# Kernel optimization log

Measured on AMD Instinct MI355X. Metric: run time of the kernel, lower is better.

## Reference

```python
import jax, jax.numpy as jnp
import numpy as np

DIM_IN = 1024
DIM_OUT = 1024


def setup_inputs() -> dict:
    key = jax.random.key(0)
    k1, k2, k3, k4 = jax.random.split(key, 4)
    X = jax.random.normal(k1, (4, 2048, DIM_IN), dtype=jnp.float32)
    s = 1.0 / np.sqrt(DIM_IN)
    Wq = jax.random.normal(k2, (DIM_IN, DIM_OUT), dtype=jnp.float32) * s
    Wk = jax.random.normal(k3, (DIM_IN, DIM_OUT), dtype=jnp.float32) * s
    Wv = jax.random.normal(k4, (DIM_IN, DIM_OUT), dtype=jnp.float32) * s
    return {"X": X, "Wq": Wq, "Wk": Wk, "Wv": Wv}


def reference(X, Wq, Wk, Wv):
    # X: [B, T, Din]; projections (qkv_bias=False)
    q = jnp.einsum('btd,de->bte', X, Wq)   # [B, T, Dout]
    k = jnp.einsum('btd,de->bte', X, Wk)
    v = jnp.einsum('btd,de->bte', X, Wv)
    T = X.shape[1]
    scores = jnp.einsum('bqe,bke->bqk', q, k)  # [B, T, T]
    causal = jnp.tril(jnp.ones((T, T), dtype=bool))  # mask upper triangle (future)
    scores = jnp.where(causal, scores, -jnp.inf)
    # scale=True: divide by sqrt(d); -inf stays -inf so order vs mask is irrelevant
    scores = scores / jnp.sqrt(jnp.asarray(k.shape[-1], dtype=scores.dtype))
    weights = jax.nn.softmax(scores, axis=-1)
    # dropout p=0.0 -> identity
    return jnp.einsum('bqk,bke->bqe', weights, v)
```

## Files before the change

### kernel.cpp

```cpp
#include <hip/hip_runtime.h>
#include <hip/hip_bf16.h>

typedef unsigned short u16;
typedef __bf16 bf16x8 __attribute__((ext_vector_type(8)));
typedef float f32x4 __attribute__((ext_vector_type(4)));
typedef unsigned short u16x8 __attribute__((ext_vector_type(8)));
typedef unsigned short u16x4 __attribute__((ext_vector_type(4)));

__device__ __forceinline__ float bf2f(u16 u) {
  unsigned int x = ((unsigned int)u) << 16;
  return __builtin_bit_cast(float, x);
}
__device__ __forceinline__ u16 f2bf(float f) {
  unsigned int x = __builtin_bit_cast(unsigned int, f);
  x = x + 0x7FFFu + ((x >> 16) & 1u);
  return (u16)(x >> 16);
}

__device__ __forceinline__ void gload_lds16(const u16* g, u16* l) {
  __builtin_amdgcn_global_load_lds(
      (const __attribute__((address_space(1))) unsigned int*)(unsigned long long)(uintptr_t)g,
      (__attribute__((address_space(3))) unsigned int*)(unsigned int)(uintptr_t)l,
      16, 0, 0);
}

__global__ __launch_bounds__(256) void prep_kernel(const float* __restrict__ X,
                                                   const float* __restrict__ Wq,
                                                   const float* __restrict__ Wk,
                                                   const float* __restrict__ Wv,
                                                   u16* __restrict__ Xb,
                                                   u16* __restrict__ Wt) {
  const int id = blockIdx.x;
  const int tid = threadIdx.x;
  if (id < 4096) {
    long i = ((long)id * 256 + tid) * 8;
    float4 a = *reinterpret_cast<const float4*>(X + i);
    float4 b = *reinterpret_cast<const float4*>(X + i + 4);
    u16x8 o;
    o[0] = f2bf(a.x); o[1] = f2bf(a.y); o[2] = f2bf(a.z); o[3] = f2bf(a.w);
    o[4] = f2bf(b.x); o[5] = f2bf(b.y); o[6] = f2bf(b.z); o[7] = f2bf(b.w);
    *reinterpret_cast<u16x8*>(Xb + i) = o;
    return;
  }
  __shared__ u16 t[64][72];
  const int id2 = id - 4096;
  const int z = id2 >> 8;
  const float* W = (z == 0) ? Wq : (z == 1) ? Wk : Wv;
  const float scale = (z == 0) ? (1.0f / 32.0f) : 1.0f;
  u16* out = Wt + (long)z * 1048576;
  const int c0 = (id2 & 15) * 64;
  const int r0 = ((id2 >> 4) & 15) * 64;
#pragma unroll
  for (int i = 0; i < 4; ++i) {
    int slot = tid + 256 * i;
    int lr = slot >> 4;
    int lc4 = slot & 15;
    float4 v = *reinterpret_cast<const float4*>(W + (long)(r0 + lr) * 1024 + c0 + lc4 * 4);
    t[lr][lc4 * 4 + 0] = f2bf(v.x * scale);
    t[lr][lc4 * 4 + 1] = f2bf(v.y * scale);
    t[lr][lc4 * 4 + 2] = f2bf(v.z * scale);
    t[lr][lc4 * 4 + 3] = f2bf(v.w * scale);
  }
  __syncthreads();
#pragma unroll
  for (int i = 0; i < 2; ++i) {
    int slot = tid + 256 * i;
    int orow = slot >> 3;
    int oc = slot & 7;
    u16x8 o;
#pragma unroll
    for (int j = 0; j < 8; ++j) o[j] = t[oc * 8 + j][orow];
    *reinterpret_cast<u16x8*>(out + (long)(c0 + orow) * 1024 + r0 + oc * 8) = o;
  }
}

template <int MODE>
__global__ __launch_bounds__(512, 2) void gemm_nt(const u16* __restrict__ Ag,
                                                  const u16* __restrict__ Bg,
                                                  void* __restrict__ Cg,
                                                  float* __restrict__ Sums,
                                                  int K, long sA, long sB, long sC) {
  int bm, bn, bz;
  if constexpr (MODE == 0) {
    const int id = blockIdx.x;
    const int xcd = id & 7, j = id >> 3;
    const int cx = xcd & 1, cy = xcd >> 1;
    bn = cx * 12 + j % 12;
    bm = cy * 16 + j / 12;
    bz = 0;
  } else if constexpr (MODE == 1) {
    const int id = blockIdx.y * 16 + blockIdx.x;
    const int xcd = id & 7, j = id >> 3;
    bn = j & 15;
    bm = (j >> 4) ? (15 - xcd) : xcd;
    bz = blockIdx.z;
    if (bn > bm) return;
  } else {
    const int id = blockIdx.y * 8 + blockIdx.x;
    const int xcd = id & 7, j = id >> 3;
    bn = j & 7;
    bm = (j >> 3) ? (15 - xcd) : xcd;
    bz = blockIdx.z;
  }

  const u16* A = Ag + (long)bz * sA;
  const u16* B = Bg + (long)bz * sB;
  const int m0 = bm * 128, n0 = bn * 128;
  int kEnd = K;
  if constexpr (MODE == 2) kEnd = m0 + 128;

  __shared__ u16 ldsA[2][8192];
  __shared__ u16 ldsB[2][8192];

  const int tid = threadIdx.x;
  const int lane = tid & 63;
  const int wid = tid >> 6;
  const int wm = wid >> 2, wn = wid & 3;
  const int l16 = lane & 15, lh = lane >> 4;
  const int strow = tid >> 3;
  const int scol = ((tid & 7) ^ (strow & 7)) * 8;
  const int rsw = l16 & 7;

  bool vblk = false;
  if constexpr (MODE == 0) vblk = ((bn >> 3) == 2);

  f32x4 acc[4][2];
#pragma unroll
  for (int mi = 0; mi < 4; ++mi)
#pragma unroll
    for (int ni = 0; ni < 2; ++ni) acc[mi][ni] = (f32x4)(0.0f);

  auto stage = [&](int d, int k0) {
#pragma unroll
    for (int l = 0; l < 2; ++l) {
      const int row = l * 64 + strow;
      gload_lds16(A + (long)(m0 + row) * K + k0 + scol, &ldsA[d][l * 4096 + tid * 8]);
      gload_lds16(B + (long)(n0 + row) * K + k0 + scol, &ldsB[d][l * 4096 + tid * 8]);
    }
  };

  stage(0, 0);
  int cur = 0;
  for (int k0 = 0; k0 < kEnd; k0 += 64) {
    __syncthreads();
    if (k0 + 64 < kEnd) stage(cur ^ 1, k0 + 64);
#pragma unroll
    for (int kk = 0; kk < 2; ++kk) {
      bf16x8 af[4], bfr[2];
#pragma unroll
      for (int mi = 0; mi < 4; ++mi)
        af[mi] = *reinterpret_cast<const bf16x8*>(
            &ldsA[cur][(wm * 64 + mi * 16 + l16) * 64 + (((kk * 4 + lh) ^ rsw)) * 8]);
#pragma unroll
      for (int ni = 0; ni < 2; ++ni)
        bfr[ni] = *reinterpret_cast<const bf16x8*>(
            &ldsB[cur][(wn * 32 + ni * 16 + l16) * 64 + (((kk * 4 + lh) ^ rsw)) * 8]);
      if (!vblk) {
#pragma unroll
        for (int mi = 0; mi < 4; ++mi)
#pragma unroll
          for (int ni = 0; ni < 2; ++ni)
            acc[mi][ni] = __builtin_amdgcn_mfma_f32_16x16x32_bf16(bfr[ni], af[mi], acc[mi][ni], 0, 0, 0);
      } else {
#pragma unroll
        for (int mi = 0; mi < 4; ++mi)
#pragma unroll
          for (int ni = 0; ni < 2; ++ni)
            acc[mi][ni] = __builtin_amdgcn_mfma_f32_16x16x32_bf16(af[mi], bfr[ni], acc[mi][ni], 0, 0, 0);
      }
    }
    cur ^= 1;
  }

  if constexpr (MODE == 0) {
    const int z = bn >> 3;
    const int colbase = (bn & 7) * 128;
    if (z < 2) {
      u16* C = (u16*)Cg + (long)z * 8388608;
      const long rown = (long)(m0 + wm * 64 + l16);
      const int coln = colbase + wn * 32 + lh * 4;
#pragma unroll
      for (int mi = 0; mi < 4; ++mi)
#pragma unroll
        for (int ni = 0; ni < 2; ++ni) {
          u16x4 o;
#pragma unroll
          for (int r = 0; r < 4; ++r) o[r] = f2bf(acc[mi][ni][r]);
          *reinterpret_cast<u16x4*>(&C[(rown + mi * 16) * 1024 + coln + ni * 16]) = o;
        }
    } else {
      u16* C = (u16*)Cg + 16777216;
      const int b = m0 >> 11;
      const int t0 = (m0 & 2047) + wm * 64 + lh * 4;
      const int e0 = colbase + wn * 32 + l16;
#pragma unroll
      for (int mi = 0; mi < 4; ++mi)
#pragma unroll
        for (int ni = 0; ni < 2; ++ni) {
          u16x4 o;
#pragma unroll
          for (int r = 0; r < 4; ++r) o[r] = f2bf(acc[mi][ni][r]);
          *reinterpret_cast<u16x4*>(
              &C[(long)b * 2097152 + (long)(e0 + ni * 16) * 2048 + t0 + mi * 16]) = o;
        }
    }
  } else if constexpr (MODE == 1) {
    u16* C = (u16*)Cg + (long)bz * sC;
    float* sums = Sums + (long)bz * 2048;
    const long rown = (long)(m0 + wm * 64 + l16);
    const int coln = n0 + wn * 32 + lh * 4;
#pragma unroll
    for (int mi = 0; mi < 4; ++mi) {
      const int gr = m0 + wm * 64 + l16 + mi * 16;
      float rs = 0.0f;
#pragma unroll
      for (int ni = 0; ni < 2; ++ni) {
        u16x4 o;
#pragma unroll
        for (int r = 0; r < 4; ++r) {
          const int gc = coln + ni * 16 + r;
          const float e = (gc <= gr) ? __expf(acc[mi][ni][r]) : 0.0f;
          const u16 ub = f2bf(e);
          o[r] = ub;
          rs += bf2f(ub);
        }
        *reinterpret_cast<u16x4*>(&C[(rown + mi * 16) * 2048 + coln + ni * 16]) = o;
      }
      rs += __shfl_xor(rs, 16);
      rs += __shfl_xor(rs, 32);
      if (lh == 0) atomicAdd(&sums[gr], rs);
    }
  } else {
    float* C = (float*)Cg + (long)bz * sC;
    const float* sums = Sums + (long)bz * 2048;
    const long rown = (long)(m0 + wm * 64 + l16);
    const int coln = n0 + wn * 32 + lh * 4;
#pragma unroll
    for (int mi = 0; mi < 4; ++mi) {
      const float inv = 1.0f / sums[(int)rown + mi * 16];
#pragma unroll
      for (int ni = 0; ni < 2; ++ni) {
        f32x4 v = acc[mi][ni] * inv;
        *reinterpret_cast<f32x4*>(&C[(rown + mi * 16) * 1024 + coln + ni * 16]) = v;
      }
    }
  }
}

extern "C" void kernel_launch(void* const* d_in, const int* in_sizes, int n_in,
                              void* d_out, int out_size, void* d_ws, size_t ws_size,
                              hipStream_t stream) {
  const float* X  = (const float*)d_in[0];
  const float* Wq = (const float*)d_in[1];
  const float* Wk = (const float*)d_in[2];
  const float* Wv = (const float*)d_in[3];

  u16* Xb = (u16*)d_ws;
  u16* Wt = Xb + 8388608;
  u16* Qb = Wt + 3145728;
  u16* Kb = Qb + 8388608;
  u16* Vt = Kb + 8388608;
  u16* S  = Vt + 8388608;
  float* sums = (float*)(S + 16777216);

  hipMemsetAsync(sums, 0, 4 * 2048 * sizeof(float), stream);

  prep_kernel<<<4864, 256, 0, stream>>>(X, Wq, Wk, Wv, Xb, Wt);

  gemm_nt<0><<<1536, 512, 0, stream>>>(Xb, Wt, Qb, nullptr, 1024, 0L, 0L, 0L);

  gemm_nt<1><<<dim3(16, 16, 4), 512, 0, stream>>>(
      Qb, Kb, S, sums, 1024, 2097152L, 2097152L, 4194304L);

  gemm_nt<2><<<dim3(8, 16, 4), 512, 0, stream>>>(
      S, Vt, (float*)d_out, sums, 2048, 4194304L, 2097152L, 2097152L);
}
```

Before: 145.8 us.

## Replace the QKV projection GEMM with a dedicated 128x192-tile kernel

A new gemm_qkv kernel computes the fused Q/K/V projection with 128x192 output tiles (three 16-wide N fragments per wave) and 1024 blocks instead of 1536 blocks of 128x128. The aim is more operand reuse per staged tile and a grid that fills the GPU in fewer rounds. The MODE 0 path, including its swapped-operand transposed V store, is removed from gemm_nt. V is now written to its transposed layout with scalar 2-byte stores, which may coalesce worse. Launch bounds of (512,4) raise register pressure, with a risk of spills.

```diff
diff --git a/kernel.cpp b/kernel.cpp
--- a/kernel.cpp
+++ b/kernel.cpp
@@ -74,6 +74,99 @@
   }
 }
 
+__global__ __launch_bounds__(512, 4) void gemm_qkv(const u16* __restrict__ Xb,
+                                                   const u16* __restrict__ Wt,
+                                                   u16* __restrict__ Qb,
+                                                   u16* __restrict__ Vt) {
+  const int id = blockIdx.x;
+  const int xcd = id & 7, j = id >> 3;
+  const int bn = (xcd & 1) * 8 + (j & 7);
+  const int bm = ((xcd >> 1) << 4) + (j >> 3);
+  const int m0 = bm * 128, n0 = bn * 192;
+  const int K = 1024;
+
+  __shared__ u16 ldsA[2][8192];
+  __shared__ u16 ldsB[2][12288];
+
+  const int tid = threadIdx.x;
+  const int lane = tid & 63;
+  const int wid = tid >> 6;
+  const int wm = wid >> 2, wn = wid & 3;
+  const int l16 = lane & 15, lh = lane >> 4;
+  const int strow = tid >> 3;
+  const int scol = ((tid & 7) ^ (strow & 7)) * 8;
+  const int rsw = l16 & 7;
+
+  f32x4 acc[4][3];
+#pragma unroll
+  for (int mi = 0; mi < 4; ++mi)
+#pragma unroll
+    for (int ni = 0; ni < 3; ++ni) acc[mi][ni] = (f32x4)(0.0f);
+
+  auto stage = [&](int d, int k0) {
+#pragma unroll
+    for (int l = 0; l < 2; ++l)
+      gload_lds16(Xb + (long)(m0 + l * 64 + strow) * K + k0 + scol,
+                  &ldsA[d][l * 4096 + tid * 8]);
+#pragma unroll
+    for (int l = 0; l < 3; ++l)
+      gload_lds16(Wt + (long)(n0 + l * 64 + strow) * K + k0 + scol,
+                  &ldsB[d][l * 4096 + tid * 8]);
+  };
+
+  stage(0, 0);
+  int cur = 0;
+  for (int k0 = 0; k0 < K; k0 += 64) {
+    __syncthreads();
+    if (k0 + 64 < K) stage(cur ^ 1, k0 + 64);
+#pragma unroll
+    for (int kk = 0; kk < 2; ++kk) {
+      bf16x8 af[4], bfr[3];
+#pragma unroll
+      for (int mi = 0; mi < 4; ++mi)
+        af[mi] = *reinterpret_cast<const bf16x8*>(
+            &ldsA[cur][(wm * 64 + mi * 16 + l16) * 64 + (((kk * 4 + lh) ^ rsw)) * 8]);
+#pragma unroll
+      for (int ni = 0; ni < 3; ++ni)
+        bfr[ni] = *reinterpret_cast<const bf16x8*>(
+            &ldsB[cur][(wn * 48 + ni * 16 + l16) * 64 + (((kk * 4 + lh) ^ rsw)) * 8]);
+#pragma unroll
+      for (int mi = 0; mi < 4; ++mi)
+#pragma unroll
+        for (int ni = 0; ni < 3; ++ni)
+          acc[mi][ni] = __builtin_amdgcn_mfma_f32_16x16x32_bf16(bfr[ni], af[mi], acc[mi][ni], 0, 0, 0);
+    }
+    cur ^= 1;
+  }
+
+  const int rowt = m0 + wm * 64 + l16;
+#pragma unroll
+  for (int ni = 0; ni < 3; ++ni) {
+    const int gc0 = n0 + wn * 48 + ni * 16 + lh * 4;
+    const int z = gc0 >> 10;
+    const int lc = gc0 & 1023;
+    if (z < 2) {
+      u16* C = Qb + (long)z * 8388608;
+#pragma unroll
+      for (int mi = 0; mi < 4; ++mi) {
+        u16x4 o;
+#pragma unroll
+        for (int r = 0; r < 4; ++r) o[r] = f2bf(acc[mi][ni][r]);
+        *reinterpret_cast<u16x4*>(&C[(long)(rowt + mi * 16) * 1024 + lc]) = o;
+      }
+    } else {
+#pragma unroll
+      for (int mi = 0; mi < 4; ++mi) {
+        const int grow = rowt + mi * 16;
+        const int b = grow >> 11, t = grow & 2047;
+#pragma unroll
+        for (int r = 0; r < 4; ++r)
+          Vt[(long)b * 2097152 + (long)(lc + r) * 2048 + t] = f2bf(acc[mi][ni][r]);
+      }
+    }
+  }
+}
+
 template <int MODE>
 __global__ __launch_bounds__(512, 2) void gemm_nt(const u16* __restrict__ Ag,
                                                   const u16* __restrict__ Bg,
@@ -81,14 +174,7 @@
                                                   float* __restrict__ Sums,
                                                   int K, long sA, long sB, long sC) {
   int bm, bn, bz;
-  if constexpr (MODE == 0) {
-    const int id = blockIdx.x;
-    const int xcd = id & 7, j = id >> 3;
-    const int cx = xcd & 1, cy = xcd >> 1;
-    bn = cx * 12 + j % 12;
-    bm = cy * 16 + j / 12;
-    bz = 0;
-  } else if constexpr (MODE == 1) {
+  if constexpr (MODE == 1) {
     const int id = blockIdx.y * 16 + blockIdx.x;
     const int xcd = id & 7, j = id >> 3;
     bn = j & 15;
@@ -121,9 +207,6 @@
   const int scol = ((tid & 7) ^ (strow & 7)) * 8;
   const int rsw = l16 & 7;
 
-  bool vblk = false;
-  if constexpr (MODE == 0) vblk = ((bn >> 3) == 2);
-
   f32x4 acc[4][2];
 #pragma unroll
   for (int mi = 0; mi < 4; ++mi)
@@ -155,56 +238,16 @@
       for (int ni = 0; ni < 2; ++ni)
         bfr[ni] = *reinterpret_cast<const bf16x8*>(
             &ldsB[cur][(wn * 32 + ni * 16 + l16) * 64 + (((kk * 4 + lh) ^ rsw)) * 8]);
-      if (!vblk) {
-#pragma unroll
-        for (int mi = 0; mi < 4; ++mi)
-#pragma unroll
-          for (int ni = 0; ni < 2; ++ni)
-            acc[mi][ni] = __builtin_amdgcn_mfma_f32_16x16x32_bf16(bfr[ni], af[mi], acc[mi][ni], 0, 0, 0);
-      } else {
-#pragma unroll
-        for (int mi = 0; mi < 4; ++mi)
-#pragma unroll
-          for (int ni = 0; ni < 2; ++ni)
-            acc[mi][ni] = __builtin_amdgcn_mfma_f32_16x16x32_bf16(af[mi], bfr[ni], acc[mi][ni], 0, 0, 0);
-      }
+#pragma unroll
+      for (int mi = 0; mi < 4; ++mi)
+#pragma unroll
+        for (int ni = 0; ni < 2; ++ni)
+          acc[mi][ni] = __builtin_amdgcn_mfma_f32_16x16x32_bf16(bfr[ni], af[mi], acc[mi][ni], 0, 0, 0);
     }
     cur ^= 1;
   }
 
-  if constexpr (MODE == 0) {
-    const int z = bn >> 3;
-    const int colbase = (bn & 7) * 128;
-    if (z < 2) {
-      u16* C = (u16*)Cg + (long)z * 8388608;
-      const long rown = (long)(m0 + wm * 64 + l16);
-      const int coln = colbase + wn * 32 + lh * 4;
-#pragma unroll
-      for (int mi = 0; mi < 4; ++mi)
-#pragma unroll
-        for (int ni = 0; ni < 2; ++ni) {
-          u16x4 o;
-#pragma unroll
-          for (int r = 0; r < 4; ++r) o[r] = f2bf(acc[mi][ni][r]);
-          *reinterpret_cast<u16x4*>(&C[(rown + mi * 16) * 1024 + coln + ni * 16]) = o;
-        }
-    } else {
-      u16* C = (u16*)Cg + 16777216;
-      const int b = m0 >> 11;
-      const int t0 = (m0 & 2047) + wm * 64 + lh * 4;
-      const int e0 = colbase + wn * 32 + l16;
-#pragma unroll
-      for (int mi = 0; mi < 4; ++mi)
-#pragma unroll
-        for (int ni = 0; ni < 2; ++ni) {
-          u16x4 o;
-#pragma unroll
-          for (int r = 0; r < 4; ++r) o[r] = f2bf(acc[mi][ni][r]);
-          *reinterpret_cast<u16x4*>(
-              &C[(long)b * 2097152 + (long)(e0 + ni * 16) * 2048 + t0 + mi * 16]) = o;
-        }
-    }
-  } else if constexpr (MODE == 1) {
+  if constexpr (MODE == 1) {
     u16* C = (u16*)Cg + (long)bz * sC;
     float* sums = Sums + (long)bz * 2048;
     const long rown = (long)(m0 + wm * 64 + l16);
@@ -267,7 +310,7 @@
 
   prep_kernel<<<4864, 256, 0, stream>>>(X, Wq, Wk, Wv, Xb, Wt);
 
-  gemm_nt<0><<<1536, 512, 0, stream>>>(Xb, Wt, Qb, nullptr, 1024, 0L, 0L, 0L);
+  gemm_qkv<<<1024, 512, 0, stream>>>(Xb, Wt, Qb, Vt);
 
   gemm_nt<1><<<dim3(16, 16, 4), 512, 0, stream>>>(
       Qb, Kb, S, sums, 1024, 2097152L, 2097152L, 4194304L);
```

Result: faster. 139.0 us (-4.6%).
